# Optimization experiments

Measured on AMD Instinct MI355X. Metric: run time of the kernel, lower is better.

The kernel has to match this reference:

```python
import jax, jax.numpy as jnp
import numpy as np

BS, M = 256, 64            # batch, tokens per sample (8x8 latent grid)
NUM_EMB = 1024             # codebook size
LATENT = 1024              # latent_channel (== NUM_EMB, forced by the .view in the original)
GRID = 8                   # 8x8 spatial layout of the M=64 tokens


def setup_inputs() -> dict:
    key = jax.random.key(0)
    k1, k2 = jax.random.split(key)
    encoding_indices = jax.random.randint(k1, (BS, M), 0, NUM_EMB, dtype=jnp.int64)
    weight = jax.random.normal(k2, (NUM_EMB, LATENT), dtype=jnp.float32)  # embedding table
    return {"encoding_indices": encoding_indices, "weight": weight}


def reference(encoding_indices, weight):
    # Original: one-hot scatter [bs*M, NUM_EMB] @ weight -> exact same values as a gather,
    # since each one-hot row selects exactly one codebook row. We use the efficient gather.
    bs, m = encoding_indices.shape
    c = weight.shape[1]
    quantized = jnp.take(weight, encoding_indices.reshape(-1), axis=0)      # [bs*M, C]
    quantized = quantized.reshape(bs, GRID, GRID, c)                         # .view(bs, 8, 8, C)
    quantized = jnp.transpose(quantized, (0, 3, 1, 2))                       # .permute(0,3,1,2)
    return quantized                                                          # [bs, C, 8, 8]
```

## Files before the change

### kernel.cpp

```cpp
#include <hip/hip_runtime.h>
#include <hip/hip_bf16.h>


#define BS   256
#define M    64
#define C    1024
#define PAD  65

typedef float fx4 __attribute__((ext_vector_type(4)));

__global__ __launch_bounds__(256) void gather_transpose_kernel(
    const int* __restrict__ idx,
    const float* __restrict__ w,
    float* __restrict__ out)
{
    const int b  = blockIdx.x >> 4;
    const int c0 = (blockIdx.x & 15) << 6;

    __shared__ int   s_idx[M];
    __shared__ float tile[M * PAD];

    const int t = threadIdx.x;
    if (t < M) s_idx[t] = idx[b * M + t];
    __syncthreads();

    const int f = t & 15;
#pragma unroll
    for (int j = 0; j < 4; ++j) {
        const int m   = (t >> 4) + (j << 4);
        const int row = s_idx[m];
        const fx4 v = *(const fx4*)(w + row * C + c0 + (f << 2));
        tile[((f << 2) + 0) * PAD + m] = v.x;
        tile[((f << 2) + 1) * PAD + m] = v.y;
        tile[((f << 2) + 2) * PAD + m] = v.z;
        tile[((f << 2) + 3) * PAD + m] = v.w;
    }
    __syncthreads();

    float* obase = out + (((size_t)(b * C + c0)) << 6);
#pragma unroll
    for (int j = 0; j < 4; ++j) {
        const int fo = (j << 8) + t;
        const int cc = fo >> 4;
        const int m  = (fo & 15) << 2;
        fx4 v;
        v.x = tile[cc * PAD + m + 0];
        v.y = tile[cc * PAD + m + 1];
        v.z = tile[cc * PAD + m + 2];
        v.w = tile[cc * PAD + m + 3];
        __builtin_nontemporal_store(v, (fx4*)(obase + (cc << 6) + m));
    }
}

extern "C" void kernel_launch(void* const* d_in, const int* in_sizes, int n_in,
                              void* d_out, int out_size, void* d_ws, size_t ws_size,
                              hipStream_t stream) {
    const int*   idx = (const int*)d_in[0];
    const float* w   = (const float*)d_in[1];
    float*       out = (float*)d_out;

    dim3 grid(BS * (C / 64));
    dim3 block(256);
    gather_transpose_kernel<<<grid, block, 0, stream>>>(idx, w, out);
}
```

Before: 79.81 us.

## Process four channel tiles per block with double-buffered LDS gather/store pipeline

Each block now handles four 64-channel tiles instead of one, cutting the grid from 4096 to 1024 blocks. The index load is shared across the tiles, and a double-buffered LDS tile lets the gather loads for the next tile be issued before the transposed stores of the current tile. The aim is to overlap global reads with writes and amortize per-block setup. The cost is double the LDS per block and fewer blocks, which can lower occupancy and parallelism for this memory-bound op.

```diff
diff --git a/kernel.cpp b/kernel.cpp
--- a/kernel.cpp
+++ b/kernel.cpp
@@ -2,10 +2,11 @@
 #include <hip/hip_bf16.h>
 
 
-#define BS   256
-#define M    64
-#define C    1024
-#define PAD  65
+#define BS    256
+#define M     64
+#define C     1024
+#define PAD   65
+#define TILES 4
 
 typedef float fx4 __attribute__((ext_vector_type(4)));
 
@@ -14,42 +15,73 @@
     const float* __restrict__ w,
     float* __restrict__ out)
 {
-    const int b  = blockIdx.x >> 4;
-    const int c0 = (blockIdx.x & 15) << 6;
+    const int b      = blockIdx.x >> 2;
+    const int c_base = (blockIdx.x & 3) << 8;
 
     __shared__ int   s_idx[M];
-    __shared__ float tile[M * PAD];
+    __shared__ float tile[2][M * PAD];
 
     const int t = threadIdx.x;
     if (t < M) s_idx[t] = idx[b * M + t];
     __syncthreads();
 
-    const int f = t & 15;
+    const int f  = t & 15;
+    const int m0 = t >> 4;
+
+    const float* wrow[4];
 #pragma unroll
-    for (int j = 0; j < 4; ++j) {
-        const int m   = (t >> 4) + (j << 4);
-        const int row = s_idx[m];
-        const fx4 v = *(const fx4*)(w + row * C + c0 + (f << 2));
-        tile[((f << 2) + 0) * PAD + m] = v.x;
-        tile[((f << 2) + 1) * PAD + m] = v.y;
-        tile[((f << 2) + 2) * PAD + m] = v.z;
-        tile[((f << 2) + 3) * PAD + m] = v.w;
+    for (int j = 0; j < 4; ++j)
+        wrow[j] = w + (size_t)s_idx[m0 + (j << 4)] * C + c_base + (f << 2);
+
+    float* const obase = out + (((size_t)b * C + c_base) << 6);
+
+#define GATHER(ti, vv)                                            \
+    _Pragma("unroll")                                             \
+    for (int j = 0; j < 4; ++j)                                   \
+        vv[j] = *(const fx4*)(wrow[j] + ((ti) << 6));
+
+#define LDSWRITE(buf, vv)                                         \
+    _Pragma("unroll")                                             \
+    for (int j = 0; j < 4; ++j) {                                 \
+        const int mm = m0 + (j << 4);                             \
+        tile[buf][((f << 2) + 0) * PAD + mm] = vv[j].x;           \
+        tile[buf][((f << 2) + 1) * PAD + mm] = vv[j].y;           \
+        tile[buf][((f << 2) + 2) * PAD + mm] = vv[j].z;           \
+        tile[buf][((f << 2) + 3) * PAD + mm] = vv[j].w;           \
+    }
+
+#define STORE(buf, ti)                                            \
+    _Pragma("unroll")                                             \
+    for (int j = 0; j < 4; ++j) {                                 \
+        const int fo = (j << 8) + t;                              \
+        const int cc = fo >> 4;                                   \
+        const int mm = (fo & 15) << 2;                            \
+        fx4 o;                                                    \
+        o.x = tile[buf][cc * PAD + mm + 0];                       \
+        o.y = tile[buf][cc * PAD + mm + 1];                       \
+        o.z = tile[buf][cc * PAD + mm + 2];                       \
+        o.w = tile[buf][cc * PAD + mm + 3];                       \
+        __builtin_nontemporal_store(                              \
+            o, (fx4*)(obase + ((ti) << 12) + (cc << 6) + mm));    \
+    }
+
+    {
+        fx4 v[4];
+        GATHER(0, v);
+        LDSWRITE(0, v);
     }
     __syncthreads();
 
-    float* obase = out + (((size_t)(b * C + c0)) << 6);
 #pragma unroll
-    for (int j = 0; j < 4; ++j) {
-        const int fo = (j << 8) + t;
-        const int cc = fo >> 4;
-        const int m  = (fo & 15) << 2;
-        fx4 v;
-        v.x = tile[cc * PAD + m + 0];
-        v.y = tile[cc * PAD + m + 1];
-        v.z = tile[cc * PAD + m + 2];
-        v.w = tile[cc * PAD + m + 3];
-        __builtin_nontemporal_store(v, (fx4*)(obase + (cc << 6) + m));
+    for (int ti = 0; ti < TILES - 1; ++ti) {
+        fx4 v[4];
+        GATHER(ti + 1, v);
+        STORE(ti & 1, ti);
+        LDSWRITE((ti + 1) & 1, v);
+        __syncthreads();
     }
+
+    STORE((TILES - 1) & 1, TILES - 1);
 }
 
 extern "C" void kernel_launch(void* const* d_in, const int* in_sizes, int n_in,
@@ -59,7 +91,7 @@
     const float* w   = (const float*)d_in[1];
     float*       out = (float*)d_out;
 
-    dim3 grid(BS * (C / 64));
+    dim3 grid(BS * TILES);
     dim3 block(256);
     gather_transpose_kernel<<<grid, block, 0, stream>>>(idx, w, out);
 }
```

Result: slower. 83.00 us (+4.0%).
